# Optimization experiments

Hardware: AMD Instinct MI355X
Metric: run time of the kernel (lower is better)

The kernel has to match this reference:

```python
import jax, jax.numpy as jnp
import numpy as np

N = 100000
E = 1250000
D = 64
K = 3
A_COEF = 1.0
B_COEF = 1.0
L_DOM = -1.0
R_DOM = 1.0


def setup_inputs() -> dict:
    key = jax.random.key(0)
    k1, k2, k3, k4, k5 = jax.random.split(key, 5)
    x = jax.random.normal(k1, (N, D), dtype=jnp.float32)
    edge_index = jax.random.randint(k2, (2, E), 0, N, dtype=jnp.int64)
    edge_weight = jax.random.uniform(k3, (E,), dtype=jnp.float32)
    alpha_params = jnp.ones((K + 1,), dtype=jnp.float32)
    lin_w = jax.random.normal(k4, ((K + 1) * D, D), dtype=jnp.float32) / np.sqrt((K + 1) * D)
    lin_b = jnp.zeros((D,), dtype=jnp.float32)
    return {"x": x, "edge_index": edge_index, "edge_weight": edge_weight,
            "alpha_params": alpha_params, "lin_w": lin_w, "lin_b": lin_b}


def reference(x, edge_index, edge_weight, alpha_params, lin_w, lin_b):
    row, col = edge_index[0], edge_index[1]
    # gcn normalization: deg from source nodes, deg<0.5 -> +1
    deg = jax.ops.segment_sum(jnp.ones((E,), x.dtype), row, num_segments=N)
    deg = jnp.where(deg < 0.5, deg + 1.0, deg)
    dis = deg ** -0.5
    val = dis[row] * edge_weight * dis[col]  # [E]

    def spmm(h):  # adj @ h : out[row] += val * h[col]
        return jax.ops.segment_sum(val[:, None] * h[col], row, num_segments=N)

    alphas = jnp.tanh(alpha_params)  # basealpha = 1.0
    a, b, l, r = A_COEF, B_COEF, L_DOM, R_DOM
    xs = [x]
    for L in range(1, K + 1):
        Ax = spmm(xs[-1])
        if L == 1:
            coef1 = (a - b) / 2 - (a + b + 2) / 2 * ((l + r) / (r - l))
            coef2 = (a + b + 2) / (r - l)
            nxt = alphas[0] * (coef1 * xs[-1] + coef2 * Ax)
        else:
            coef_l = 2 * L * (L + a + b) * (2 * L - 2 + a + b)
            coef_lm1_1 = (2 * L + a + b - 1) * (2 * L + a + b) * (2 * L + a + b - 2)
            coef_lm1_2 = (2 * L + a + b - 1) * (a ** 2 - b ** 2)
            coef_lm2 = 2 * (L - 1 + a) * (L - 1 + b) * (2 * L + a + b)
            tmp1 = alphas[L - 1] * (coef_lm1_1 / coef_l)
            tmp2 = alphas[L - 1] * (coef_lm1_2 / coef_l)
            tmp3 = alphas[L - 1] * alphas[L - 2] * (coef_lm2 / coef_l)
            tmp1_2 = tmp1 * (2.0 / (r - l))
            tmp2_2 = tmp1 * ((r + l) / (r - l)) + tmp2
            nxt = tmp1_2 * Ax - tmp2_2 * xs[-1] - tmp3 * xs[-2]
        xs.append(nxt)
    x_cat = jnp.concatenate(xs, axis=1)  # [N, (K+1)*D]
    return x_cat @ lin_w + lin_b
```

## Files before the change

kernel.cpp:

```cpp
#include <hip/hip_runtime.h>
#include <hip/hip_bf16.h>
#include <math.h>

#define NN 100000
#define EE 1250000
#define DD 64

typedef __attribute__((ext_vector_type(8))) short short8;
typedef __attribute__((ext_vector_type(8))) unsigned short u16x8;
typedef __attribute__((ext_vector_type(4))) float f32x4;

__device__ __forceinline__ unsigned short f2b(float f) {
    unsigned u = __float_as_uint(f);
    u += 0x7fffu + ((u >> 16) & 1u);
    return (unsigned short)(u >> 16);
}
__device__ __forceinline__ float b2f(unsigned short h) {
    return __uint_as_float(((unsigned)h) << 16);
}

__global__ __launch_bounds__(256) void scan_a(const int* __restrict__ degi,
                                              int* __restrict__ rowStart,
                                              int* __restrict__ bs, int N) {
    __shared__ int s[256];
    int tid = threadIdx.x;
    int i = blockIdx.x * 256 + tid;
    int v = (i < N) ? degi[i] : 0;
    s[tid] = v;
    __syncthreads();
    for (int off = 1; off < 256; off <<= 1) {
        int t = (tid >= off) ? s[tid - off] : 0;
        __syncthreads();
        s[tid] += t;
        __syncthreads();
    }
    if (i < N) rowStart[i] = s[tid] - v;
    if (tid == 255) bs[blockIdx.x] = s[255];
}

__global__ __launch_bounds__(512) void scan_b(int* __restrict__ bs, int nb) {
    __shared__ int s[512];
    int tid = threadIdx.x;
    int v = (tid < nb) ? bs[tid] : 0;
    s[tid] = v;
    __syncthreads();
    for (int off = 1; off < 512; off <<= 1) {
        int t = (tid >= off) ? s[tid - off] : 0;
        __syncthreads();
        s[tid] += t;
        __syncthreads();
    }
    if (tid < nb) bs[tid] = s[tid] - v;
}

__global__ __launch_bounds__(256) void scan_c(int* __restrict__ rowStart,
                                              const int* __restrict__ bs,
                                              int N, int E) {
    int i = blockIdx.x * 256 + threadIdx.x;
    if (i < N) rowStart[i] += bs[blockIdx.x];
    if (i == 0) rowStart[N] = E;
}

__global__ __launch_bounds__(256) void dis_kernel(const int* __restrict__ degi,
                                                  float* __restrict__ dis, int N) {
    int i = blockIdx.x * 256 + threadIdx.x;
    if (i >= N) return;
    int d = degi[i];
    float df = (d == 0) ? 1.0f : (float)d;
    dis[i] = 1.0f / sqrtf(df);
}

#define NSL 125
#define SLR 800
#define NSEG 16
#define SEGCAP 768
#define CPAD 16
#define NCB 13
#define VSCL (1.0f / 32768.0f)
__global__ __launch_bounds__(256) void binA(const int* __restrict__ row,
                                            const int* __restrict__ col,
                                            const float* __restrict__ w,
                                            uint2* __restrict__ sbuf,
                                            int* __restrict__ segCnt, int E4) {
    __shared__ int cnt[NSL];
    __shared__ int base[NSL];
    int tid = threadIdx.x;
    if (tid < NSL) cnt[tid] = 0;
    __syncthreads();
    int g = blockIdx.x & (NSEG - 1);
    int i4 = blockIdx.x * 256 + tid;
    bool act = (i4 < E4);
    int4 r4, c4;
    float4 w4;
    int sl[4], loc[4], rk[4];
    unsigned evp[4];
    if (act) {
        r4 = ((const int4*)row)[i4];
        c4 = ((const int4*)col)[i4];
        w4 = ((const float4*)w)[i4];
        int rr[4] = {r4.x, r4.y, r4.z, r4.w};
        int cc[4] = {c4.x, c4.y, c4.z, c4.w};
        float ww[4] = {w4.x, w4.y, w4.z, w4.w};
        #pragma unroll
        for (int k = 0; k < 4; ++k) {
            int r = rr[k], c = cc[k];
            int wq = (int)(ww[k] * 32768.0f + 0.5f);
            wq = (wq > 32767) ? 32767 : wq;
            evp[k] = ((unsigned)c << 15) | (unsigned)wq;
            rk[k] = r;
            sl[k] = r / SLR;
            loc[k] = atomicAdd(&cnt[sl[k]], 1);
        }
    }
    __syncthreads();
    if (tid < NSL) {
        int c = cnt[tid];
        if (c) base[tid] = atomicAdd(&segCnt[(tid * NSEG + g) * CPAD], c);
    }
    __syncthreads();
    if (act) {
        #pragma unroll
        for (int k = 0; k < 4; ++k) {
            int p = base[sl[k]] + loc[k];
            if (p < SEGCAP)
                sbuf[(size_t)(sl[k] * NSEG + g) * SEGCAP + p] =
                    make_uint2(evp[k], (unsigned)rk[k]);
        }
    }
}

__global__ __launch_bounds__(512) void deg_slice(const uint2* __restrict__ sbuf,
                                                 const int* __restrict__ segCnt,
                                                 int* __restrict__ degi) {
    __shared__ int dcnt[SLR];
    __shared__ int scnt[NSEG];
    int tid = threadIdx.x;
    int s = blockIdx.x;
    int r0 = s * SLR;
    for (int i = tid; i < SLR; i += 512) dcnt[i] = 0;
    if (tid < NSEG) {
        int c = segCnt[(s * NSEG + tid) * CPAD];
        scnt[tid] = (c > SEGCAP) ? SEGCAP : c;
    }
    __syncthreads();
    for (int slot = tid * 4; slot < NSEG * SEGCAP; slot += 2048) {
        int g = slot / SEGCAP;
        int off = slot - g * SEGCAP;
        int cg = scnt[g];
        if (off >= cg) continue;
        const uint2* seg = sbuf + (size_t)(s * NSEG + g) * SEGCAP;
        uint4 a = *(const uint4*)(seg + off);
        uint4 b = *(const uint4*)(seg + off + 2);
        atomicAdd(&dcnt[(int)a.y - r0], 1);
        if (off + 1 < cg) atomicAdd(&dcnt[(int)a.w - r0], 1);
        if (off + 2 < cg) atomicAdd(&dcnt[(int)b.y - r0], 1);
        if (off + 3 < cg) atomicAdd(&dcnt[(int)b.w - r0], 1);
    }
    __syncthreads();
    for (int i = tid; i < SLR; i += 512) {
        int gr = r0 + i;
        if (gr < NN) degi[gr] = dcnt[i];
    }
}

__global__ __launch_bounds__(512) void binB(const uint2* __restrict__ sbuf,
                                            const int* __restrict__ segCnt,
                                            const int* __restrict__ rowStart,
                                            const float* __restrict__ dis,
                                            unsigned* __restrict__ ev) {
    __shared__ int cnt2[SLR][NCB];
    __shared__ int rs[SLR];
    __shared__ float dsl[SLR];
    __shared__ int scnt[NSEG];
    int tid = threadIdx.x;
    int s = blockIdx.x;
    int r0 = s * SLR;
    for (int i = tid; i < SLR; i += 512) {
        int gr = r0 + i;
        rs[i] = (gr < NN) ? rowStart[gr] : 0;
        dsl[i] = (gr < NN) ? dis[gr] : 1.0f;
        #pragma unroll
        for (int b = 0; b < NCB; ++b) cnt2[i][b] = 0;
    }
    if (tid < NSEG) {
        int c = segCnt[(s * NSEG + tid) * CPAD];
        scnt[tid] = (c > SEGCAP) ? SEGCAP : c;
    }
    __syncthreads();
    for (int slot = tid * 4; slot < NSEG * SEGCAP; slot += 2048) {
        int g = slot / SEGCAP;
        int off = slot - g * SEGCAP;
        int cg = scnt[g];
        if (off >= cg) continue;
        const uint2* seg = sbuf + (size_t)(s * NSEG + g) * SEGCAP;
        uint4 a = *(const uint4*)(seg + off);
        uint4 b = *(const uint4*)(seg + off + 2);
        unsigned pk[4] = {a.x, a.z, b.x, b.z};
        unsigned rr[4] = {a.y, a.w, b.y, b.w};
        int nv = cg - off;
        nv = (nv > 4) ? 4 : nv;
        #pragma unroll 4
        for (int k = 0; k < 4; ++k) {
            if (k >= nv) break;
            atomicAdd(&cnt2[(int)rr[k] - r0][(pk[k] >> 15) >> 13], 1);
        }
    }
    __syncthreads();
    for (int i = tid; i < SLR; i += 512) {
        int run = rs[i];
        #pragma unroll
        for (int b = 0; b < NCB; ++b) {
            int t = cnt2[i][b];
            cnt2[i][b] = run;
            run += t;
        }
    }
    __syncthreads();
    for (int slot = tid * 4; slot < NSEG * SEGCAP; slot += 2048) {
        int g = slot / SEGCAP;
        int off = slot - g * SEGCAP;
        int cg = scnt[g];
        if (off >= cg) continue;
        const uint2* seg = sbuf + (size_t)(s * NSEG + g) * SEGCAP;
        uint4 a = *(const uint4*)(seg + off);
        uint4 b = *(const uint4*)(seg + off + 2);
        unsigned pk[4] = {a.x, a.z, b.x, b.z};
        unsigned rr[4] = {a.y, a.w, b.y, b.w};
        int nv = cg - off;
        nv = (nv > 4) ? 4 : nv;
        #pragma unroll 4
        for (int k = 0; k < 4; ++k) {
            if (k >= nv) break;
            int rl = (int)rr[k] - r0;
            int c = (int)(pk[k] >> 15);
            float wv = (float)(pk[k] & 0x7fffu) * VSCL;
            float v = dsl[rl] * wv * dis[c];
            int vq = (int)(v * 32768.0f + 0.5f);
            vq = (vq > 32767) ? 32767 : vq;
            int pos = atomicAdd(&cnt2[rl][c >> 13], 1);
            ev[pos] = ((unsigned)c << 15) | (unsigned)vq;
        }
    }
}

__global__ void coef_kernel(const float* __restrict__ ap, float* __restrict__ coef) {
    if (threadIdx.x != 0 || blockIdx.x != 0) return;
    const float a = 1.0f, b = 1.0f, l = -1.0f, r = 1.0f;
    float als[3];
    als[0] = tanhf(ap[0]);
    als[1] = tanhf(ap[1]);
    als[2] = tanhf(ap[2]);
    float coef1 = (a - b) * 0.5f - (a + b + 2.0f) * 0.5f * ((l + r) / (r - l));
    float coef2 = (a + b + 2.0f) / (r - l);
    coef[0] = als[0] * coef1;
    coef[1] = als[0] * coef2;
    for (int L = 2; L <= 3; ++L) {
        float Lf = (float)L;
        float coef_l     = 2.0f * Lf * (Lf + a + b) * (2.0f * Lf - 2.0f + a + b);
        float coef_lm1_1 = (2.0f * Lf + a + b - 1.0f) * (2.0f * Lf + a + b) * (2.0f * Lf + a + b - 2.0f);
        float coef_lm1_2 = (2.0f * Lf + a + b - 1.0f) * (a * a - b * b);
        float coef_lm2   = 2.0f * (Lf - 1.0f + a) * (Lf - 1.0f + b) * (2.0f * Lf + a + b);
        float tmp1   = als[L - 1] * (coef_lm1_1 / coef_l);
        float tmp2   = als[L - 1] * (coef_lm1_2 / coef_l);
        float tmp3   = als[L - 1] * als[L - 2] * (coef_lm2 / coef_l);
        float tmp1_2 = tmp1 * (2.0f / (r - l));
        float tmp2_2 = tmp1 * ((r + l) / (r - l)) + tmp2;
        int base = 2 + (L - 2) * 3;
        coef[base + 0] = tmp1_2;
        coef[base + 1] = tmp2_2;
        coef[base + 2] = tmp3;
    }
}

__global__ __launch_bounds__(256) void tobf16(const float4* __restrict__ in,
                                              ushort4* __restrict__ outb, int n4) {
    int i = blockIdx.x * 256 + threadIdx.x;
    if (i >= n4) return;
    float4 v = in[i];
    ushort4 o;
    o.x = f2b(v.x); o.y = f2b(v.y); o.z = f2b(v.z); o.w = f2b(v.w);
    outb[i] = o;
}

__global__ __launch_bounds__(256) void wt_kernel(const float* __restrict__ W,
                                                 unsigned short* __restrict__ Wt) {
    int idx = blockIdx.x * 256 + threadIdx.x;
    int n = idx >> 8, k = idx & 255;
    Wt[idx] = f2b(W[k * 64 + n]);
}

__device__ __forceinline__ void fma8(float* a, unsigned u, u16x8 h) {
    float v = (float)(u & 0x7fffu) * VSCL;
    #pragma unroll
    for (int c = 0; c < 8; ++c) a[c] += v * b2f(h[c]);
}

template <int MODE>
__global__ __launch_bounds__(256) void spmm_fused(const int* __restrict__ rowStart,
                                                  const unsigned* __restrict__ ev,
                                                  const unsigned short* __restrict__ hb,
                                                  const unsigned short* __restrict__ xm1,
                                                  const unsigned short* __restrict__ xm2,
                                                  unsigned short* __restrict__ outb,
                                                  const float* __restrict__ coef,
                                                  int cbase, int N) {
    int t = blockIdx.x * 256 + threadIdx.x;
    int r = t >> 3;
    if (r >= N) return;
    int q = t & 7;
    int s0 = rowStart[r];
    int s1 = rowStart[r + 1];
    float a[8];
    #pragma unroll
    for (int c = 0; c < 8; ++c) a[c] = 0.f;
    int j = s0;
    for (; j + 7 < s1; j += 8) {
        unsigned u[8];
        u16x8 h[8];
        #pragma unroll
        for (int k = 0; k < 8; ++k) u[k] = ev[j + k];
        #pragma unroll
        for (int k = 0; k < 8; ++k)
            h[k] = *(const u16x8*)&hb[(size_t)(u[k] >> 15) * 64 + q * 8];
        #pragma unroll
        for (int k = 0; k < 8; ++k) fma8(a, u[k], h[k]);
    }
    for (; j + 3 < s1; j += 4) {
        unsigned u0 = ev[j];
        unsigned u1 = ev[j + 1];
        unsigned u2 = ev[j + 2];
        unsigned u3 = ev[j + 3];
        u16x8 h0 = *(const u16x8*)&hb[(size_t)(u0 >> 15) * 64 + q * 8];
        u16x8 h1 = *(const u16x8*)&hb[(size_t)(u1 >> 15) * 64 + q * 8];
        u16x8 h2 = *(const u16x8*)&hb[(size_t)(u2 >> 15) * 64 + q * 8];
        u16x8 h3 = *(const u16x8*)&hb[(size_t)(u3 >> 15) * 64 + q * 8];
        fma8(a, u0, h0);
        fma8(a, u1, h1);
        fma8(a, u2, h2);
        fma8(a, u3, h3);
    }
    for (; j < s1; ++j) {
        unsigned u0 = ev[j];
        u16x8 h0 = *(const u16x8*)&hb[(size_t)(u0 >> 15) * 64 + q * 8];
        fma8(a, u0, h0);
    }
    size_t oi = (size_t)r * 64 + q * 8;
    float o[8];
    if (MODE == 0) {
        float c0 = coef[cbase], c1 = coef[cbase + 1];
        u16x8 m1 = *(const u16x8*)&xm1[oi];
        #pragma unroll
        for (int c = 0; c < 8; ++c) o[c] = c0 * b2f(m1[c]) + c1 * a[c];
    } else {
        float c0 = coef[cbase], c1 = coef[cbase + 1], c2 = coef[cbase + 2];
        u16x8 m1 = *(const u16x8*)&xm1[oi];
        u16x8 m2 = *(const u16x8*)&xm2[oi];
        #pragma unroll
        for (int c = 0; c < 8; ++c)
            o[c] = c0 * a[c] - c1 * b2f(m1[c]) - c2 * b2f(m2[c]);
    }
    u16x8 ob;
    #pragma unroll
    for (int c = 0; c < 8; ++c) ob[c] = f2b(o[c]);
    *(u16x8*)&outb[oi] = ob;
}

__global__ __launch_bounds__(256, 4) void final_gemm_mfma(
        const ushort4* __restrict__ x0,
        const ushort4* __restrict__ x1,
        const ushort4* __restrict__ x2,
        const ushort4* __restrict__ x3,
        const unsigned short* __restrict__ Wt,
        const float* __restrict__ bias,
        float* __restrict__ out) {
    const int tid = threadIdx.x;
    const int lane = tid & 63;
    const int w = tid >> 6;
    const int m = lane & 15;
    const int quad = lane >> 4;
    const int n0 = (int)blockIdx.x * 128;

    int gr0 = n0 + 16 * w + m;
    int gr1 = gr0 + 64;
    size_t ar0 = (size_t)((gr0 < NN) ? gr0 : 0) * 16;
    size_t ar1 = (size_t)((gr1 < NN) ? gr1 : 0) * 16;

    f32x4 acc0[4], acc1[4];
    #pragma unroll
    for (int nt = 0; nt < 4; ++nt) {
        acc0[nt] = (f32x4){0.f, 0.f, 0.f, 0.f};
        acc1[nt] = (f32x4){0.f, 0.f, 0.f, 0.f};
    }

    #pragma unroll
    for (int ks = 0; ks < 8; ++ks) {
        const ushort4* p = (ks < 2) ? x0 : (ks < 4) ? x1 : (ks < 6) ? x2 : x3;
        size_t ko = (size_t)((ks & 1) * 8 + quad * 2);
        short8 af0 = *(const short8*)&p[ar0 + ko];
        short8 af1 = *(const short8*)&p[ar1 + ko];
        #pragma unroll
        for (int nt = 0; nt < 4; ++nt) {
            short8 bf = *(const short8*)&Wt[(nt * 16 + m) * 256 + ks * 32 + quad * 8];
            acc0[nt] = __builtin_amdgcn_mfma_f32_16x16x32_bf16(af0, bf, acc0[nt], 0, 0, 0);
            acc1[nt] = __builtin_amdgcn_mfma_f32_16x16x32_bf16(af1, bf, acc1[nt], 0, 0, 0);
        }
    }

    #pragma unroll
    for (int nt = 0; nt < 4; ++nt) {
        float bv = bias[nt * 16 + m];
        #pragma unroll
        for (int rg = 0; rg < 4; ++rg) {
            int node0 = n0 + 16 * w + quad * 4 + rg;
            int node1 = node0 + 64;
            if (node0 < NN) out[(size_t)node0 * 64 + nt * 16 + m] = acc0[nt][rg] + bv;
            if (node1 < NN) out[(size_t)node1 * 64 + nt * 16 + m] = acc1[nt][rg] + bv;
        }
    }
}

extern "C" void kernel_launch(void* const* d_in, const int* in_sizes, int n_in,
                              void* d_out, int out_size, void* d_ws, size_t ws_size,
                              hipStream_t stream) {
    const float* x  = (const float*)d_in[0];
    const int*   ei = (const int*)d_in[1];
    const float* ew = (const float*)d_in[2];
    const float* ap = (const float*)d_in[3];
    const float* lw = (const float*)d_in[4];
    const float* lb = (const float*)d_in[5];
    float* out = (float*)d_out;

    const int N = NN, E = EE;
    const int ND = N * DD;

    const int* row = ei;
    const int* col = ei + E;

    char* ws = (char*)d_ws;
    ushort4* xb = (ushort4*)ws;
    ushort4* Ab = (ushort4*)(ws + (size_t)ND * 2);
    ushort4* Bb = (ushort4*)(ws + (size_t)ND * 4);
    ushort4* Cb = (ushort4*)(ws + (size_t)ND * 6);
    uint2*   sbuf   = (uint2*)(ws + (size_t)ND * 4);
    int*     segCnt = (int*)(ws + (size_t)ND * 6);
    unsigned* ev = (unsigned*)(ws + (size_t)ND * 8);
    char* sm    = ws + (size_t)ND * 8 + (size_t)E * 4;
    float* coef     = (float*)sm;
    float* dis      = (float*)(sm + 256);
    int*   degi     = (int*)(sm + 256 + (size_t)N * 4);
    int*   rowStart = (int*)(sm + 256 + (size_t)N * 8);
    int*   bs       = (int*)(sm + 256 + (size_t)N * 12 + 64);
    unsigned short* Wt = (unsigned short*)(sm + 256 + (size_t)N * 12 + 64 + 4096);

    const int gridN  = (N + 255) / 256;
    const int gridSp = (N * 8) / 256;
    const int gridCv = (ND / 4) / 256;
    const int gridG  = (N + 127) / 128;
    const int E4     = E / 4;
    const int gridA  = (E4 + 255) / 256;

    hipMemsetAsync(segCnt, 0, (size_t)NSL * NSEG * CPAD * 4, stream);
    coef_kernel<<<1, 64, 0, stream>>>(ap, coef);
    wt_kernel<<<64, 256, 0, stream>>>(lw, Wt);
    binA<<<gridA, 256, 0, stream>>>(row, col, ew, sbuf, segCnt, E4);
    deg_slice<<<NSL, 512, 0, stream>>>(sbuf, segCnt, degi);
    scan_a<<<gridN, 256, 0, stream>>>(degi, rowStart, bs, N);
    scan_b<<<1, 512, 0, stream>>>(bs, gridN);
    scan_c<<<gridN, 256, 0, stream>>>(rowStart, bs, N, E);
    dis_kernel<<<gridN, 256, 0, stream>>>(degi, dis, N);
    binB<<<NSL, 512, 0, stream>>>(sbuf, segCnt, rowStart, dis, ev);

    tobf16<<<gridCv, 256, 0, stream>>>((const float4*)x, xb, ND / 4);

    spmm_fused<0><<<gridSp, 256, 0, stream>>>(rowStart, ev,
                                              (const unsigned short*)xb,
                                              (const unsigned short*)xb,
                                              (const unsigned short*)xb,
                                              (unsigned short*)Ab, coef, 0, N);
    spmm_fused<1><<<gridSp, 256, 0, stream>>>(rowStart, ev,
                                              (const unsigned short*)Ab,
                                              (const unsigned short*)Ab,
                                              (const unsigned short*)xb,
                                              (unsigned short*)Bb, coef, 2, N);
    spmm_fused<1><<<gridSp, 256, 0, stream>>>(rowStart, ev,
                                              (const unsigned short*)Bb,
                                              (const unsigned short*)Bb,
                                              (const unsigned short*)Ab,
                                              (unsigned short*)Cb, coef, 5, N);

    final_gemm_mfma<<<gridG, 256, 0, stream>>>(xb, Ab, Bb, Cb, Wt, lb, out);
}
```

Before: 258.2 us.

## Process SpMM rows in column-bucket order with two rows per thread group

binB now writes per-row, per-column-bucket start offsets into a new rs2 array, which adds extra global writes. The SpMM kernel uses these offsets to walk each row bucket by bucket. Each 8-thread group handles two rows at once, interleaving their gathers so that concurrently running rows touch the same column range of the feature matrix for better cache locality. The inner loops lose the old 8/4-way unrolling, and the 14 offset loads per row add overhead; the launch bound changes to 6 waves.

```diff
diff --git a/kernel.cpp b/kernel.cpp
--- a/kernel.cpp
+++ b/kernel.cpp
@@ -167,7 +167,8 @@
                                             const int* __restrict__ segCnt,
                                             const int* __restrict__ rowStart,
                                             const float* __restrict__ dis,
-                                            unsigned* __restrict__ ev) {
+                                            unsigned* __restrict__ ev,
+                                            int* __restrict__ rs2) {
     __shared__ int cnt2[SLR][NCB];
     __shared__ int rs[SLR];
     __shared__ float dsl[SLR];
@@ -213,6 +214,12 @@
             int t = cnt2[i][b];
             cnt2[i][b] = run;
             run += t;
+        }
+        int gr = r0 + i;
+        if (gr < NN) {
+            #pragma unroll
+            for (int b = 0; b < NCB; ++b) rs2[b * NN + gr] = cnt2[i][b];
+            rs2[13 * NN + gr] = run;
         }
     }
     __syncthreads();
@@ -296,73 +303,68 @@
 }
 
 template <int MODE>
-__global__ __launch_bounds__(256) void spmm_fused(const int* __restrict__ rowStart,
-                                                  const unsigned* __restrict__ ev,
-                                                  const unsigned short* __restrict__ hb,
-                                                  const unsigned short* __restrict__ xm1,
-                                                  const unsigned short* __restrict__ xm2,
-                                                  unsigned short* __restrict__ outb,
-                                                  const float* __restrict__ coef,
-                                                  int cbase, int N) {
-    int t = blockIdx.x * 256 + threadIdx.x;
-    int r = t >> 3;
-    if (r >= N) return;
-    int q = t & 7;
-    int s0 = rowStart[r];
-    int s1 = rowStart[r + 1];
-    float a[8];
-    #pragma unroll
-    for (int c = 0; c < 8; ++c) a[c] = 0.f;
-    int j = s0;
-    for (; j + 7 < s1; j += 8) {
-        unsigned u[8];
-        u16x8 h[8];
-        #pragma unroll
-        for (int k = 0; k < 8; ++k) u[k] = ev[j + k];
-        #pragma unroll
-        for (int k = 0; k < 8; ++k)
-            h[k] = *(const u16x8*)&hb[(size_t)(u[k] >> 15) * 64 + q * 8];
-        #pragma unroll
-        for (int k = 0; k < 8; ++k) fma8(a, u[k], h[k]);
-    }
-    for (; j + 3 < s1; j += 4) {
-        unsigned u0 = ev[j];
-        unsigned u1 = ev[j + 1];
-        unsigned u2 = ev[j + 2];
-        unsigned u3 = ev[j + 3];
-        u16x8 h0 = *(const u16x8*)&hb[(size_t)(u0 >> 15) * 64 + q * 8];
-        u16x8 h1 = *(const u16x8*)&hb[(size_t)(u1 >> 15) * 64 + q * 8];
-        u16x8 h2 = *(const u16x8*)&hb[(size_t)(u2 >> 15) * 64 + q * 8];
-        u16x8 h3 = *(const u16x8*)&hb[(size_t)(u3 >> 15) * 64 + q * 8];
-        fma8(a, u0, h0);
-        fma8(a, u1, h1);
-        fma8(a, u2, h2);
-        fma8(a, u3, h3);
-    }
-    for (; j < s1; ++j) {
-        unsigned u0 = ev[j];
-        u16x8 h0 = *(const u16x8*)&hb[(size_t)(u0 >> 15) * 64 + q * 8];
-        fma8(a, u0, h0);
-    }
-    size_t oi = (size_t)r * 64 + q * 8;
-    float o[8];
-    if (MODE == 0) {
-        float c0 = coef[cbase], c1 = coef[cbase + 1];
-        u16x8 m1 = *(const u16x8*)&xm1[oi];
-        #pragma unroll
-        for (int c = 0; c < 8; ++c) o[c] = c0 * b2f(m1[c]) + c1 * a[c];
-    } else {
-        float c0 = coef[cbase], c1 = coef[cbase + 1], c2 = coef[cbase + 2];
-        u16x8 m1 = *(const u16x8*)&xm1[oi];
-        u16x8 m2 = *(const u16x8*)&xm2[oi];
-        #pragma unroll
-        for (int c = 0; c < 8; ++c)
-            o[c] = c0 * a[c] - c1 * b2f(m1[c]) - c2 * b2f(m2[c]);
-    }
-    u16x8 ob;
-    #pragma unroll
-    for (int c = 0; c < 8; ++c) ob[c] = f2b(o[c]);
-    *(u16x8*)&outb[oi] = ob;
+__global__ __launch_bounds__(256, 6) void spmm_fused(const int* __restrict__ rs2,
+                                                     const unsigned* __restrict__ ev,
+                                                     const unsigned short* __restrict__ hb,
+                                                     const unsigned short* __restrict__ xm1,
+                                                     const unsigned short* __restrict__ xm2,
+                                                     unsigned short* __restrict__ outb,
+                                                     const float* __restrict__ coef,
+                                                     int cbase) {
+    const int tid = threadIdx.x;
+    const int q = tid & 7;
+    const int r0 = (int)blockIdx.x * 64 + (tid >> 3) * 2;
+    const int r1 = r0 + 1;
+    const bool v0 = (r0 < NN), v1 = (r1 < NN);
+
+    float a0[8], a1[8];
+    #pragma unroll
+    for (int c = 0; c < 8; ++c) { a0[c] = 0.f; a1[c] = 0.f; }
+
+    int e0 = v0 ? rs2[r0] : 0;
+    int e1 = v1 ? rs2[r1] : 0;
+
+    #pragma unroll 1
+    for (int cb = 1; cb <= NCB; ++cb) {
+        int n0 = v0 ? rs2[cb * NN + r0] : 0;
+        int n1 = v1 ? rs2[cb * NN + r1] : 0;
+        for (; e0 < n0; ++e0) {
+            unsigned u = ev[e0];
+            u16x8 h = *(const u16x8*)&hb[(size_t)(u >> 15) * 64 + q * 8];
+            fma8(a0, u, h);
+        }
+        for (; e1 < n1; ++e1) {
+            unsigned u = ev[e1];
+            u16x8 h = *(const u16x8*)&hb[(size_t)(u >> 15) * 64 + q * 8];
+            fma8(a1, u, h);
+        }
+    }
+
+    #pragma unroll
+    for (int rr = 0; rr < 2; ++rr) {
+        int r = (rr == 0) ? r0 : r1;
+        if (r >= NN) continue;
+        const float* a = (rr == 0) ? a0 : a1;
+        size_t oi = (size_t)r * 64 + q * 8;
+        float o[8];
+        if (MODE == 0) {
+            float c0 = coef[cbase], c1 = coef[cbase + 1];
+            u16x8 m1 = *(const u16x8*)&xm1[oi];
+            #pragma unroll
+            for (int c = 0; c < 8; ++c) o[c] = c0 * b2f(m1[c]) + c1 * a[c];
+        } else {
+            float c0 = coef[cbase], c1 = coef[cbase + 1], c2 = coef[cbase + 2];
+            u16x8 m1 = *(const u16x8*)&xm1[oi];
+            u16x8 m2 = *(const u16x8*)&xm2[oi];
+            #pragma unroll
+            for (int c = 0; c < 8; ++c)
+                o[c] = c0 * a[c] - c1 * b2f(m1[c]) - c2 * b2f(m2[c]);
+        }
+        u16x8 ob;
+        #pragma unroll
+        for (int c = 0; c < 8; ++c) ob[c] = f2b(o[c]);
+        *(u16x8*)&outb[oi] = ob;
+    }
 }
 
 __global__ __launch_bounds__(256, 4) void final_gemm_mfma(
@@ -451,9 +453,10 @@
     int*   rowStart = (int*)(sm + 256 + (size_t)N * 8);
     int*   bs       = (int*)(sm + 256 + (size_t)N * 12 + 64);
     unsigned short* Wt = (unsigned short*)(sm + 256 + (size_t)N * 12 + 64 + 4096);
+    int*   rs2      = (int*)(sm + 2097152);
 
     const int gridN  = (N + 255) / 256;
-    const int gridSp = (N * 8) / 256;
+    const int gridSp = (N + 63) / 64;
     const int gridCv = (ND / 4) / 256;
     const int gridG  = (N + 127) / 128;
     const int E4     = E / 4;
@@ -468,25 +471,25 @@
     scan_b<<<1, 512, 0, stream>>>(bs, gridN);
     scan_c<<<gridN, 256, 0, stream>>>(rowStart, bs, N, E);
     dis_kernel<<<gridN, 256, 0, stream>>>(degi, dis, N);
-    binB<<<NSL, 512, 0, stream>>>(sbuf, segCnt, rowStart, dis, ev);
+    binB<<<NSL, 512, 0, stream>>>(sbuf, segCnt, rowStart, dis, ev, rs2);
 
     tobf16<<<gridCv, 256, 0, stream>>>((const float4*)x, xb, ND / 4);
 
-    spmm_fused<0><<<gridSp, 256, 0, stream>>>(rowStart, ev,
+    spmm_fused<0><<<gridSp, 256, 0, stream>>>(rs2, ev,
                                               (const unsigned short*)xb,
                                               (const unsigned short*)xb,
                                               (const unsigned short*)xb,
-                                              (unsigned short*)Ab, coef, 0, N);
-    spmm_fused<1><<<gridSp, 256, 0, stream>>>(rowStart, ev,
+                                              (unsigned short*)Ab, coef, 0);
+    spmm_fused<1><<<gridSp, 256, 0, stream>>>(rs2, ev,
                                               (const unsigned short*)Ab,
                                               (const unsigned short*)Ab,
                                               (const unsigned short*)xb,
-                                              (unsigned short*)Bb, coef, 2, N);
-    spmm_fused<1><<<gridSp, 256, 0, stream>>>(rowStart, ev,
+                                              (unsigned short*)Bb, coef, 2);
+    spmm_fused<1><<<gridSp, 256, 0, stream>>>(rs2, ev,
                                               (const unsigned short*)Bb,
                                               (const unsigned short*)Bb,
                                               (const unsigned short*)Ab,
-                                              (unsigned short*)Cb, coef, 5, N);
+                                              (unsigned short*)Cb, coef, 5);
 
     final_gemm_mfma<<<gridG, 256, 0, stream>>>(xb, Ab, Bb, Cb, Wt, lb, out);
 }
```

Result: slower. 345.0 us (+33.6%).
